# Performance work log

Measured on AMD Instinct MI355X. Metric: run time of the kernel, lower is better.

The kernel has to match this reference:

```python
import jax, jax.numpy as jnp
import numpy as np

IN_F, OUT_F, N_TOK = 4096, 4096, 8192

def setup_inputs() -> dict:
    key = jax.random.key(0)
    k1, k2, k3, k4, k5 = jax.random.split(key, 5)
    bound = 1.0 / np.sqrt(IN_F)  # kaiming_uniform-ish scale for mean, uniform for bias
    x = jax.random.normal(k1, (N_TOK, IN_F), dtype=jnp.float32)
    mean = jax.random.uniform(k2, (OUT_F, IN_F), minval=-bound, maxval=bound, dtype=jnp.float32)
    sigma = jax.random.uniform(k3, (OUT_F, IN_F), minval=0.05, maxval=0.2, dtype=jnp.float32)
    bias = jax.random.uniform(k4, (OUT_F,), minval=-bound, maxval=bound, dtype=jnp.float32)
    # uniform[-1, 1] noise matrix (torch init.uniform_(w, a=-1, b=1))
    noise = jax.random.uniform(k5, (OUT_F, IN_F), minval=-1.0, maxval=1.0, dtype=jnp.float32)
    sigma_mult = 2  # discrete bucket multiplier in {1, 2, 4}
    return {"x": x, "mean": mean, "sigma": sigma, "bias": bias, "noise": noise, "sigma_mult": sigma_mult}

def reference(x, mean, sigma, bias, noise, sigma_mult):
    # w = mean * (1 + noise * |sigma| * sigma_mult), then F.linear(x, w, bias) = x @ w.T + bias
    w = mean * (1.0 + noise * jnp.abs(sigma) * sigma_mult)  # [out, in]
    return jnp.einsum('ti,oi->to', x, w) + bias
```

## Files before the change

kernel.cpp:

```cpp
#include <hip/hip_runtime.h>
#include <hip/hip_bf16.h>

#define M_TOK 8192
#define N_OUT 4096
#define K_IN  4096

typedef __attribute__((ext_vector_type(8))) short bf16x8;
typedef __attribute__((ext_vector_type(16))) float f32x16;
typedef unsigned short u16;

__device__ static inline u16 f2bf(float f) {
    union { float f; unsigned int u; } v; v.f = f;
    unsigned int u = v.u;
    u += 0x7FFFu + ((u >> 16) & 1u);
    return (u16)(u >> 16);
}

__device__ static inline void load_lds16(const void* g, void* l) {
    __builtin_amdgcn_global_load_lds(
        (const __attribute__((address_space(1))) unsigned int*)g,
        (__attribute__((address_space(3))) unsigned int*)l,
        16, 0, 0);
}

__global__ void prep_kernel(const float* __restrict__ x,
                            const float* __restrict__ mean,
                            const float* __restrict__ sigma,
                            const float* __restrict__ noise,
                            const int* __restrict__ smult,
                            u16* __restrict__ xb, u16* __restrict__ wb) {
    if (blockIdx.x < 2048) {
        const int n4 = (M_TOK * K_IN) / 4;
        int i = blockIdx.x * blockDim.x + threadIdx.x;
        const int stride = 2048 * 256;
        for (int e = i; e < n4; e += stride) {
            float4 v = reinterpret_cast<const float4*>(x)[e];
            ushort4 o;
            o.x = f2bf(v.x); o.y = f2bf(v.y); o.z = f2bf(v.z); o.w = f2bf(v.w);
            reinterpret_cast<ushort4*>(xb)[e] = o;
        }
    } else {
        const float sm = (float)(*smult);
        const int n4 = (N_OUT * K_IN) / 4;
        int i = (blockIdx.x - 2048) * blockDim.x + threadIdx.x;
        const int stride = 1024 * 256;
        for (int e = i; e < n4; e += stride) {
            float4 m = reinterpret_cast<const float4*>(mean)[e];
            float4 s = reinterpret_cast<const float4*>(sigma)[e];
            float4 z = reinterpret_cast<const float4*>(noise)[e];
            ushort4 o;
            o.x = f2bf(m.x * (1.0f + z.x * fabsf(s.x) * sm));
            o.y = f2bf(m.y * (1.0f + z.y * fabsf(s.y) * sm));
            o.z = f2bf(m.z * (1.0f + z.z * fabsf(s.z) * sm));
            o.w = f2bf(m.w * (1.0f + z.w * fabsf(s.w) * sm));
            reinterpret_cast<ushort4*>(wb)[e] = o;
        }
    }
}


#define BAR()    __builtin_amdgcn_s_barrier()
#define SCHED0() __builtin_amdgcn_sched_barrier(0)
#define VMC4()  asm volatile("s_waitcnt vmcnt(4)" ::: "memory")
#define VMC2()  asm volatile("s_waitcnt vmcnt(2)" ::: "memory")
#define VMC0()  asm volatile("s_waitcnt vmcnt(0)" ::: "memory")

#define LD_A(DST, PAIR, AB) \
  _Pragma("unroll") for (int mt_ = 0; mt_ < 2; ++mt_) \
  _Pragma("unroll") for (int kc_ = 0; kc_ < 4; ++kc_) \
    DST[mt_][kc_] = *reinterpret_cast<const bf16x8*>( \
      (AB) + (((PAIR)*2 + mt_)*32 + r31)*64 + koffE[kc_]);

#define LD_B(DST, NTT, BB) \
  _Pragma("unroll") for (int kc_ = 0; kc_ < 4; ++kc_) \
    DST[kc_] = *reinterpret_cast<const bf16x8*>( \
      (BB) + ((NTT)*32 + r31)*64 + koffE[kc_]);

#define OCT(MP, NTT, AR, BR) \
  __builtin_amdgcn_s_setprio(1); \
  _Pragma("unroll") for (int kc_ = 0; kc_ < 4; ++kc_) \
  _Pragma("unroll") for (int mt_ = 0; mt_ < 2; ++mt_) \
    acc[(MP)*2 + mt_][NTT] = __builtin_amdgcn_mfma_f32_32x32x16_bf16( \
      AR[mt_][kc_], BR[kc_], acc[(MP)*2 + mt_][NTT], 0, 0, 0); \
  __builtin_amdgcn_s_setprio(0);

#define STAGE_A(T, H, BUF) { \
  const u16* g_ = Abase + (size_t)((H)*128 + srow) * K_IN + (T)*64 + sxcol; \
  load_lds16(g_, smem + (BUF)*32768 + (H)*8192 + tid*8); \
  load_lds16(g_ + (size_t)64*K_IN, smem + (BUF)*32768 + (H)*8192 + 4096 + tid*8); }

#define STAGE_B(T, H, BUF) { \
  const u16* g_ = Bbase + (size_t)((H)*128 + srow) * K_IN + (T)*64 + sxcol; \
  load_lds16(g_, smem + (BUF)*32768 + 16384 + (H)*8192 + tid*8); \
  load_lds16(g_ + (size_t)64*K_IN, smem + (BUF)*32768 + 16384 + (H)*8192 + 4096 + tid*8); }

__global__ __launch_bounds__(512, 2)
void gemm_bias_kernel(const u16* __restrict__ A, const u16* __restrict__ B,
                      const float* __restrict__ bias, float* __restrict__ C) {
    __shared__ u16 smem[65536];

    const int tid  = threadIdx.x;
    const int lane = tid & 63;
    const int wid  = tid >> 6;
    const int wm   = wid >> 2;
    const int wn   = wid & 3;
    const int r31  = lane & 31;
    const int hi5  = lane >> 5;
    const int xr   = lane & 7;

    const int bid = blockIdx.x;
    const int xcd = bid & 7;
    const int c   = bid >> 3;
    const int r   = c >> 5;
    const int s   = c & 31;
    const int bm  = xcd * 4 + (s & 3);
    const int bn  = r * 8 + (s >> 2);
    const int brow = bm * 256;
    const int bcol = bn * 256;

    const u16* Abase = A + (size_t)brow * K_IN;
    const u16* Bbase = B + (size_t)bcol * K_IN;

    const int srow  = tid >> 3;
    const int sxcol = ((tid & 7) ^ (srow & 7)) * 8;

    int koffE[4];
    #pragma unroll
    for (int kc = 0; kc < 4; ++kc)
        koffE[kc] = ((kc * 2 + hi5) ^ xr) * 8;

    const u16* A0 = smem +         wm * 8192;
    const u16* A1 = smem + 32768 + wm * 8192;
    const u16* B0 = smem +         16384 + (wn >> 1) * 8192 + (wn & 1) * 4096;
    const u16* B1 = smem + 32768 + 16384 + (wn >> 1) * 8192 + (wn & 1) * 4096;

    f32x16 acc[4][2];
    #pragma unroll
    for (int m = 0; m < 4; ++m)
        #pragma unroll
        for (int n = 0; n < 2; ++n)
            #pragma unroll
            for (int e = 0; e < 16; ++e)
                acc[m][n][e] = 0.f;

    bf16x8 aRe[2][4], aRo[2][4], bA0[4], bA1[4], bB[4];

    STAGE_B(0, 0, 0); STAGE_B(0, 1, 0);
    STAGE_A(0, 0, 0); STAGE_A(0, 1, 0);
    STAGE_B(1, 0, 1); STAGE_B(1, 1, 1);
    VMC4(); BAR();
    LD_A(aRe, 0, A0); LD_B(bA0, 0, B0);

    for (int i = 0; i < 31; ++i) {
        const int t1 = 2 * i + 1, t2 = 2 * i + 2, t3 = 2 * i + 3;
        LD_B(bB, 1, B0); STAGE_A(t1, 0, 1);
        SCHED0(); OCT(0, 0, aRe, bA0); BAR();
        LD_A(aRo, 1, A0); STAGE_A(t1, 1, 1);
        SCHED0(); OCT(0, 1, aRe, bB); BAR();
        STAGE_B(t2, 0, 0);
        SCHED0(); OCT(1, 1, aRo, bB); VMC2(); BAR();
        LD_A(aRe, 0, A1); LD_B(bA1, 0, B1); STAGE_B(t2, 1, 0);
        SCHED0(); OCT(1, 0, aRo, bA0); BAR();
        LD_B(bB, 1, B1); STAGE_A(t2, 0, 0);
        SCHED0(); OCT(0, 0, aRe, bA1); BAR();
        LD_A(aRo, 1, A1); STAGE_A(t2, 1, 0);
        SCHED0(); OCT(0, 1, aRe, bB); BAR();
        STAGE_B(t3, 0, 1);
        SCHED0(); OCT(1, 1, aRo, bB); VMC2(); BAR();
        LD_A(aRe, 0, A0); LD_B(bA0, 0, B0); STAGE_B(t3, 1, 1);
        SCHED0(); OCT(1, 0, aRo, bA1); BAR();
    }

    LD_B(bB, 1, B0); STAGE_A(63, 0, 1);
    SCHED0(); OCT(0, 0, aRe, bA0); BAR();
    LD_A(aRo, 1, A0); STAGE_A(63, 1, 1);
    SCHED0(); OCT(0, 1, aRe, bB); BAR();
    SCHED0(); OCT(1, 1, aRo, bB); VMC0(); BAR();
    LD_A(aRe, 0, A1); LD_B(bA1, 0, B1);
    SCHED0(); OCT(1, 0, aRo, bA0); BAR();
    LD_B(bB, 1, B1);
    SCHED0(); OCT(0, 0, aRe, bA1); BAR();
    LD_A(aRo, 1, A1);
    SCHED0(); OCT(0, 1, aRe, bB); BAR();
    SCHED0(); OCT(1, 1, aRo, bB); BAR();
    OCT(1, 0, aRo, bA1);

    const int crow0 = brow + wm * 128;
    const int ccol0 = bcol + wn * 64;
    #pragma unroll
    for (int nt = 0; nt < 2; ++nt) {
        const int col = ccol0 + nt * 32 + r31;
        const float bv = bias[col];
        #pragma unroll
        for (int mt = 0; mt < 4; ++mt) {
            #pragma unroll
            for (int g = 0; g < 4; ++g) {
                #pragma unroll
                for (int rr = 0; rr < 4; ++rr) {
                    const int row = crow0 + mt * 32 + g * 8 + 4 * hi5 + rr;
                    C[(size_t)row * N_OUT + col] = acc[mt][nt][g * 4 + rr] + bv;
                }
            }
        }
    }
}

extern "C" void kernel_launch(void* const* d_in, const int* in_sizes, int n_in,
                              void* d_out, int out_size, void* d_ws, size_t ws_size,
                              hipStream_t stream) {
    const float* x     = (const float*)d_in[0];
    const float* mean  = (const float*)d_in[1];
    const float* sigma = (const float*)d_in[2];
    const float* bias  = (const float*)d_in[3];
    const float* noise = (const float*)d_in[4];
    const int*   smult = (const int*)d_in[5];
    float* out = (float*)d_out;

    const size_t x_elems = (size_t)M_TOK * K_IN;
    const size_t w_elems = (size_t)N_OUT * K_IN;
    const size_t need = (x_elems + w_elems) * sizeof(u16);
    if (ws_size < need) return;

    u16* xb = (u16*)d_ws;
    u16* wb = xb + x_elems;

    prep_kernel<<<3072, 256, 0, stream>>>(x, mean, sigma, noise, smult, xb, wb);
    gemm_bias_kernel<<<512, 512, 0, stream>>>(xb, wb, bias, out);
}
```

Baseline: 329.3 us.

## Replace eight-phase ping-pong GEMM schedule with simple per-tile double buffering

Drops the hand-interleaved eight-phase main loop, which spread LDS reads, async global-to-LDS staging and MFMA groups across many barriers. In its place is a plain double-buffered loop: each K tile issues all staging for the next tile, reads its A and B fragments, runs 32 MFMAs, then waits on vmcnt(0) and a single barrier. This cuts barrier count and register-set juggling and makes the code simpler. The cost is coarser overlap: every tile waits for all outstanding global loads before continuing, and the final iteration restages tile 63 for nothing.

```diff
diff --git a/kernel.cpp b/kernel.cpp
--- a/kernel.cpp
+++ b/kernel.cpp
@@ -59,29 +59,28 @@
 }
 
 
-#define BAR()    __builtin_amdgcn_s_barrier()
+#define BARM()   { __builtin_amdgcn_s_barrier(); asm volatile("" ::: "memory"); }
 #define SCHED0() __builtin_amdgcn_sched_barrier(0)
-#define VMC4()  asm volatile("s_waitcnt vmcnt(4)" ::: "memory")
-#define VMC2()  asm volatile("s_waitcnt vmcnt(2)" ::: "memory")
-#define VMC0()  asm volatile("s_waitcnt vmcnt(0)" ::: "memory")
-
-#define LD_A(DST, PAIR, AB) \
+#define VMC0()   asm volatile("s_waitcnt vmcnt(0)" ::: "memory")
+
+#define DS_A8(PAIR, AB) \
   _Pragma("unroll") for (int mt_ = 0; mt_ < 2; ++mt_) \
   _Pragma("unroll") for (int kc_ = 0; kc_ < 4; ++kc_) \
-    DST[mt_][kc_] = *reinterpret_cast<const bf16x8*>( \
-      (AB) + (((PAIR)*2 + mt_)*32 + r31)*64 + koffE[kc_]);
-
-#define LD_B(DST, NTT, BB) \
+    aR[mt_][kc_] = *reinterpret_cast<const bf16x8*>( \
+        (AB) + ((PAIR)*64 + mt_*32 + r31)*64 + koff[kc_]);
+
+#define DS_B4(NT, BB) \
   _Pragma("unroll") for (int kc_ = 0; kc_ < 4; ++kc_) \
-    DST[kc_] = *reinterpret_cast<const bf16x8*>( \
-      (BB) + ((NTT)*32 + r31)*64 + koffE[kc_]);
-
-#define OCT(MP, NTT, AR, BR) \
+    bR[NT][kc_] = *reinterpret_cast<const bf16x8*>( \
+        (BB) + ((NT)*32 + r31)*64 + koff[kc_]);
+
+#define MX16(PAIR) \
   __builtin_amdgcn_s_setprio(1); \
   _Pragma("unroll") for (int kc_ = 0; kc_ < 4; ++kc_) \
   _Pragma("unroll") for (int mt_ = 0; mt_ < 2; ++mt_) \
-    acc[(MP)*2 + mt_][NTT] = __builtin_amdgcn_mfma_f32_32x32x16_bf16( \
-      AR[mt_][kc_], BR[kc_], acc[(MP)*2 + mt_][NTT], 0, 0, 0); \
+  _Pragma("unroll") for (int nt_ = 0; nt_ < 2; ++nt_) \
+    acc[(PAIR)*2 + mt_][nt_] = __builtin_amdgcn_mfma_f32_32x32x16_bf16( \
+        aR[mt_][kc_], bR[nt_][kc_], acc[(PAIR)*2 + mt_][nt_], 0, 0, 0); \
   __builtin_amdgcn_s_setprio(0);
 
 #define STAGE_A(T, H, BUF) { \
@@ -93,6 +92,19 @@
   const u16* g_ = Bbase + (size_t)((H)*128 + srow) * K_IN + (T)*64 + sxcol; \
   load_lds16(g_, smem + (BUF)*32768 + 16384 + (H)*8192 + tid*8); \
   load_lds16(g_ + (size_t)64*K_IN, smem + (BUF)*32768 + 16384 + (H)*8192 + 4096 + tid*8); }
+
+#define TILE(T, RB, WB) { \
+  const int tn_ = ((T) < 63) ? (T) + 1 : 63; \
+  STAGE_A(tn_, 0, WB); STAGE_A(tn_, 1, WB); \
+  STAGE_B(tn_, 0, WB); STAGE_B(tn_, 1, WB); \
+  SCHED0(); \
+  const u16* A_ = smem + (RB)*32768 + wm*8192; \
+  const u16* B_ = smem + (RB)*32768 + 16384 + wn*4096; \
+  DS_A8(0, A_); DS_B4(0, B_); DS_B4(1, B_); \
+  MX16(0); \
+  DS_A8(1, A_); \
+  MX16(1); \
+  VMC0(); BARM(); }
 
 __global__ __launch_bounds__(512, 2)
 void gemm_bias_kernel(const u16* __restrict__ A, const u16* __restrict__ B,
@@ -106,7 +118,6 @@
     const int wn   = wid & 3;
     const int r31  = lane & 31;
     const int hi5  = lane >> 5;
-    const int xr   = lane & 7;
 
     const int bid = blockIdx.x;
     const int xcd = bid & 7;
@@ -124,15 +135,10 @@
     const int srow  = tid >> 3;
     const int sxcol = ((tid & 7) ^ (srow & 7)) * 8;
 
-    int koffE[4];
+    int koff[4];
     #pragma unroll
     for (int kc = 0; kc < 4; ++kc)
-        koffE[kc] = ((kc * 2 + hi5) ^ xr) * 8;
-
-    const u16* A0 = smem +         wm * 8192;
-    const u16* A1 = smem + 32768 + wm * 8192;
-    const u16* B0 = smem +         16384 + (wn >> 1) * 8192 + (wn & 1) * 4096;
-    const u16* B1 = smem + 32768 + 16384 + (wn >> 1) * 8192 + (wn & 1) * 4096;
+        koff[kc] = ((kc * 2 + hi5) ^ (r31 & 7)) * 8;
 
     f32x16 acc[4][2];
     #pragma unroll
@@ -143,47 +149,16 @@
             for (int e = 0; e < 16; ++e)
                 acc[m][n][e] = 0.f;
 
-    bf16x8 aRe[2][4], aRo[2][4], bA0[4], bA1[4], bB[4];
-
+    bf16x8 aR[2][4], bR[2][4];
+
+    STAGE_A(0, 0, 0); STAGE_A(0, 1, 0);
     STAGE_B(0, 0, 0); STAGE_B(0, 1, 0);
-    STAGE_A(0, 0, 0); STAGE_A(0, 1, 0);
-    STAGE_B(1, 0, 1); STAGE_B(1, 1, 1);
-    VMC4(); BAR();
-    LD_A(aRe, 0, A0); LD_B(bA0, 0, B0);
-
-    for (int i = 0; i < 31; ++i) {
-        const int t1 = 2 * i + 1, t2 = 2 * i + 2, t3 = 2 * i + 3;
-        LD_B(bB, 1, B0); STAGE_A(t1, 0, 1);
-        SCHED0(); OCT(0, 0, aRe, bA0); BAR();
-        LD_A(aRo, 1, A0); STAGE_A(t1, 1, 1);
-        SCHED0(); OCT(0, 1, aRe, bB); BAR();
-        STAGE_B(t2, 0, 0);
-        SCHED0(); OCT(1, 1, aRo, bB); VMC2(); BAR();
-        LD_A(aRe, 0, A1); LD_B(bA1, 0, B1); STAGE_B(t2, 1, 0);
-        SCHED0(); OCT(1, 0, aRo, bA0); BAR();
-        LD_B(bB, 1, B1); STAGE_A(t2, 0, 0);
-        SCHED0(); OCT(0, 0, aRe, bA1); BAR();
-        LD_A(aRo, 1, A1); STAGE_A(t2, 1, 0);
-        SCHED0(); OCT(0, 1, aRe, bB); BAR();
-        STAGE_B(t3, 0, 1);
-        SCHED0(); OCT(1, 1, aRo, bB); VMC2(); BAR();
-        LD_A(aRe, 0, A0); LD_B(bA0, 0, B0); STAGE_B(t3, 1, 1);
-        SCHED0(); OCT(1, 0, aRo, bA1); BAR();
+    VMC0(); BARM();
+
+    for (int i = 0; i < 32; ++i) {
+        TILE(2 * i,     0, 1);
+        TILE(2 * i + 1, 1, 0);
     }
-
-    LD_B(bB, 1, B0); STAGE_A(63, 0, 1);
-    SCHED0(); OCT(0, 0, aRe, bA0); BAR();
-    LD_A(aRo, 1, A0); STAGE_A(63, 1, 1);
-    SCHED0(); OCT(0, 1, aRe, bB); BAR();
-    SCHED0(); OCT(1, 1, aRo, bB); VMC0(); BAR();
-    LD_A(aRe, 0, A1); LD_B(bA1, 0, B1);
-    SCHED0(); OCT(1, 0, aRo, bA0); BAR();
-    LD_B(bB, 1, B1);
-    SCHED0(); OCT(0, 0, aRe, bA1); BAR();
-    LD_A(aRo, 1, A1);
-    SCHED0(); OCT(0, 1, aRe, bB); BAR();
-    SCHED0(); OCT(1, 1, aRo, bB); BAR();
-    OCT(1, 0, aRo, bA1);
 
     const int crow0 = brow + wm * 128;
     const int ccol0 = bcol + wn * 64;
```

Result: slower. 341.2 us (+3.6%).
